# Kernel tuning notes

Hardware: AMD Instinct MI355X
Metric: run time of the kernel (lower is better)

Reference implementation:

```python
import jax, jax.numpy as jnp
import numpy as np

BETA = 0.9
THR = 1.0
NUM_STEPS = 10


@jax.custom_vjp
def spike(x):
    # Heaviside forward, fast-sigmoid surrogate backward (slope=25)
    return (x > 0).astype(x.dtype)

def _spike_fwd(x):
    return spike(x), x

def _spike_bwd(x, g):
    return (g / (25.0 * jnp.abs(x) + 1.0) ** 2,)

spike.defvjp(_spike_fwd, _spike_bwd)


def setup_inputs() -> dict:
    key = jax.random.key(0)
    ks = jax.random.split(key, 5)
    B = 65536
    x = jax.random.normal(ks[0], (B, 1, 16, 16), dtype=jnp.float32)
    conv_w = jax.random.normal(ks[1], (8, 1, 3, 3), dtype=jnp.float32) * 0.3
    conv_b = jax.random.normal(ks[2], (8,), dtype=jnp.float32) * 0.1
    fc_w = jax.random.normal(ks[3], (2, 2048), dtype=jnp.float32) * 0.05
    fc_b = jax.random.normal(ks[4], (2,), dtype=jnp.float32) * 0.1
    return {"x": x, "conv_w": conv_w, "conv_b": conv_b, "fc_w": fc_w, "fc_b": fc_b}


def reference(x, conv_w, conv_b, fc_w, fc_b):
    B = x.shape[0]
    # conv1(x) is loop-invariant (x is fed at every step) -> hoist
    cur1 = jax.lax.conv_general_dilated(
        x, conv_w, window_strides=(1, 1), padding="SAME",
        dimension_numbers=("NCHW", "OIHW", "NCHW"),
    ) + conv_b[None, :, None, None]  # [B, 8, 16, 16]

    def step(carry, _):
        mem1, mem2, acc = carry
        # snntorch Leaky: reset (detached) from previous mem, subtract mechanism
        reset1 = jax.lax.stop_gradient((mem1 > THR).astype(mem1.dtype))
        mem1 = BETA * mem1 + cur1 - reset1 * THR
        spk1 = spike(mem1 - THR)
        flat = spk1.reshape(B, -1)  # [B, 2048]
        cur2 = flat @ fc_w.T + fc_b  # [B, 2]
        reset2 = jax.lax.stop_gradient((mem2 > THR).astype(mem2.dtype))
        mem2 = BETA * mem2 + cur2 - reset2 * THR
        spk2 = spike(mem2 - THR)
        return (mem1, mem2, acc + spk2), None

    init = (
        jnp.zeros((B, 8, 16, 16), dtype=x.dtype),
        jnp.zeros((B, 2), dtype=x.dtype),
        jnp.zeros((B, 2), dtype=x.dtype),
    )
    (mem1, mem2, sum_out), _ = jax.lax.scan(step, init, None, length=NUM_STEPS)
    return sum_out
```

## Files before the change

### kernel.cpp

```cpp
#include <hip/hip_runtime.h>

#define NSTEP 10

__device__ __forceinline__ void load_row(const float* __restrict__ p, float* r) {
    const float4* q = reinterpret_cast<const float4*>(p);
    float4 a = q[0], b = q[1], c = q[2], d = q[3];
    r[0]=a.x;  r[1]=a.y;  r[2]=a.z;  r[3]=a.w;
    r[4]=b.x;  r[5]=b.y;  r[6]=b.z;  r[7]=b.w;
    r[8]=c.x;  r[9]=c.y;  r[10]=c.z; r[11]=c.w;
    r[12]=d.x; r[13]=d.y; r[14]=d.z; r[15]=d.w;
}

__global__ __launch_bounds__(256) void snn_fused_f64(
    const float* __restrict__ x,
    const float* __restrict__ conv_w,
    const float* __restrict__ conv_b,
    const float* __restrict__ fc_w,
    const float* __restrict__ fc_b,
    float* __restrict__ out,
    int B)
{
    __shared__ float2 fcw[2048];
    for (int j = threadIdx.x; j < 2048; j += 256)
        fcw[j] = make_float2(fc_w[j], fc_w[2048 + j]);
    __syncthreads();

    const int g  = blockIdx.x * 256 + threadIdx.x;
    const int b  = g >> 3;
    const int ch = g & 7;
    if (b >= B) return;

    double cw[9];
    #pragma unroll
    for (int k = 0; k < 9; ++k) cw[k] = (double)conv_w[ch * 9 + k];
    const double cb = (double)conv_b[ch];

    const float* xb = x + (size_t)b * 256;

    double sx[NSTEP], sy[NSTEP];
    #pragma unroll
    for (int t = 0; t < NSTEP; ++t) { sx[t] = 0.0; sy[t] = 0.0; }

    float r0[16], r1[16], r2[16];
    #pragma unroll
    for (int k = 0; k < 16; ++k) r0[k] = 0.f;
    load_row(xb, r1);
    load_row(xb + 16, r2);

    for (int y = 0; y < 16; ++y) {
        const int jbase = ch * 256 + y * 16;
        #pragma unroll
        for (int xx = 0; xx < 16; ++xx) {
            double c = cb;
            if (xx > 0) {
                c = fma(cw[0], (double)r0[xx - 1], c);
                c = fma(cw[3], (double)r1[xx - 1], c);
                c = fma(cw[6], (double)r2[xx - 1], c);
            }
            c = fma(cw[1], (double)r0[xx], c);
            c = fma(cw[4], (double)r1[xx], c);
            c = fma(cw[7], (double)r2[xx], c);
            if (xx < 15) {
                c = fma(cw[2], (double)r0[xx + 1], c);
                c = fma(cw[5], (double)r1[xx + 1], c);
                c = fma(cw[8], (double)r2[xx + 1], c);
            }
            const float2 w01 = fcw[jbase + xx];
            const double w0 = (double)w01.x;
            const double w1 = (double)w01.y;
            const double cm1 = c - 1.0;
            double mem = 0.0;
            bool spk = false;
            #pragma unroll
            for (int t = 0; t < NSTEP; ++t) {
                mem = fma(0.9, mem, spk ? cm1 : c);
                spk = mem > 1.0;
                sx[t] += spk ? w0 : 0.0;
                sy[t] += spk ? w1 : 0.0;
            }
        }
        #pragma unroll
        for (int k = 0; k < 16; ++k) { r0[k] = r1[k]; r1[k] = r2[k]; }
        if (y < 14) {
            load_row(xb + (y + 2) * 16, r2);
        } else {
            #pragma unroll
            for (int k = 0; k < 16; ++k) r2[k] = 0.f;
        }
    }

    #pragma unroll
    for (int t = 0; t < NSTEP; ++t) {
        sx[t] += __shfl_xor(sx[t], 1);
        sy[t] += __shfl_xor(sy[t], 1);
        sx[t] += __shfl_xor(sx[t], 2);
        sy[t] += __shfl_xor(sy[t], 2);
        sx[t] += __shfl_xor(sx[t], 4);
        sy[t] += __shfl_xor(sy[t], 4);
    }

    if (ch == 0) {
        const double fb0 = (double)fc_b[0];
        const double fb1 = (double)fc_b[1];
        double m0 = 0.0, m1 = 0.0, p0 = 0.0, p1 = 0.0;
        float a0 = 0.f, a1 = 0.f;
        #pragma unroll
        for (int t = 0; t < NSTEP; ++t) {
            m0 = fma(0.9, m0, (sx[t] + fb0) - p0);
            m1 = fma(0.9, m1, (sy[t] + fb1) - p1);
            p0 = (m0 > 1.0) ? 1.0 : 0.0;
            p1 = (m1 > 1.0) ? 1.0 : 0.0;
            a0 += (float)p0;
            a1 += (float)p1;
        }
        reinterpret_cast<float2*>(out)[b] = make_float2(a0, a1);
    }
}

extern "C" void kernel_launch(void* const* d_in, const int* in_sizes, int n_in,
                              void* d_out, int out_size, void* d_ws, size_t ws_size,
                              hipStream_t stream) {
    const float* x      = (const float*)d_in[0];
    const float* conv_w = (const float*)d_in[1];
    const float* conv_b = (const float*)d_in[2];
    const float* fc_w   = (const float*)d_in[3];
    const float* fc_b   = (const float*)d_in[4];
    float* out = (float*)d_out;

    const int B = in_sizes[0] / 256;
    const int threads = B * 8;
    const int blocks = (threads + 255) / 256;
    snn_fused_f64<<<blocks, 256, 0, stream>>>(x, conv_w, conv_b, fc_w, fc_b, out, B);
}
```

Measured before the change: 501.1 us.

## Run conv and membrane recurrence in fp32 with fp64 fallback near threshold

Moves the 3x3 conv and the 10-step membrane recurrence from fp64 to fp32, tracking a per-pixel error bound from the absolute-value sums. Pixels whose membrane comes within that bound of the threshold are flagged and recomputed in fp64 afterwards, and any differing spike bits are corrected in the fp64 accumulators. FC weights are pre-converted to double in padded shared memory so the per-step accumulation becomes a plain fma. This cuts fp64 ALU work but adds extra fp32 bound arithmetic, a rarely taken divergent fallback path, and higher register and shared-memory pressure.

```diff
diff --git a/kernel.cpp b/kernel.cpp
--- a/kernel.cpp
+++ b/kernel.cpp
@@ -1,6 +1,7 @@
 #include <hip/hip_runtime.h>
 
 #define NSTEP 10
+#define EPS32 5.9604645e-8f
 
 __device__ __forceinline__ void load_row(const float* __restrict__ p, float* r) {
     const float4* q = reinterpret_cast<const float4*>(p);
@@ -11,7 +12,7 @@
     r[12]=d.x; r[13]=d.y; r[14]=d.z; r[15]=d.w;
 }
 
-__global__ __launch_bounds__(256) void snn_fused_f64(
+__global__ __launch_bounds__(256) void snn_fused_fast(
     const float* __restrict__ x,
     const float* __restrict__ conv_w,
     const float* __restrict__ conv_b,
@@ -20,9 +21,11 @@
     float* __restrict__ out,
     int B)
 {
-    __shared__ float2 fcw[2048];
-    for (int j = threadIdx.x; j < 2048; j += 256)
-        fcw[j] = make_float2(fc_w[j], fc_w[2048 + j]);
+    __shared__ double2 fcwd[8 * 257];
+    for (int j = threadIdx.x; j < 2048; j += 256) {
+        const int c8 = j >> 8, idx = j & 255;
+        fcwd[c8 * 257 + idx] = make_double2((double)fc_w[j], (double)fc_w[2048 + j]);
+    }
     __syncthreads();
 
     const int g  = blockIdx.x * 256 + threadIdx.x;
@@ -30,12 +33,13 @@
     const int ch = g & 7;
     if (b >= B) return;
 
-    double cw[9];
-    #pragma unroll
-    for (int k = 0; k < 9; ++k) cw[k] = (double)conv_w[ch * 9 + k];
-    const double cb = (double)conv_b[ch];
+    float cw[9], aw[9];
+    #pragma unroll
+    for (int k = 0; k < 9; ++k) { cw[k] = conv_w[ch * 9 + k]; aw[k] = fabsf(cw[k]); }
+    const float cb = conv_b[ch];
 
     const float* xb = x + (size_t)b * 256;
+    const double2* fcw_ch = &fcwd[ch * 257];
 
     double sx[NSTEP], sy[NSTEP];
     #pragma unroll
@@ -48,37 +52,110 @@
     load_row(xb + 16, r2);
 
     for (int y = 0; y < 16; ++y) {
-        const int jbase = ch * 256 + y * 16;
+        unsigned rowflag = 0;
         #pragma unroll
         for (int xx = 0; xx < 16; ++xx) {
-            double c = cb;
+            float cf = cb;
+            float sa = fabsf(cb);
             if (xx > 0) {
-                c = fma(cw[0], (double)r0[xx - 1], c);
-                c = fma(cw[3], (double)r1[xx - 1], c);
-                c = fma(cw[6], (double)r2[xx - 1], c);
-            }
-            c = fma(cw[1], (double)r0[xx], c);
-            c = fma(cw[4], (double)r1[xx], c);
-            c = fma(cw[7], (double)r2[xx], c);
+                cf = fmaf(cw[0], r0[xx-1], cf); sa = fmaf(aw[0], fabsf(r0[xx-1]), sa);
+                cf = fmaf(cw[3], r1[xx-1], cf); sa = fmaf(aw[3], fabsf(r1[xx-1]), sa);
+                cf = fmaf(cw[6], r2[xx-1], cf); sa = fmaf(aw[6], fabsf(r2[xx-1]), sa);
+            }
+            cf = fmaf(cw[1], r0[xx], cf); sa = fmaf(aw[1], fabsf(r0[xx]), sa);
+            cf = fmaf(cw[4], r1[xx], cf); sa = fmaf(aw[4], fabsf(r1[xx]), sa);
+            cf = fmaf(cw[7], r2[xx], cf); sa = fmaf(aw[7], fabsf(r2[xx]), sa);
             if (xx < 15) {
-                c = fma(cw[2], (double)r0[xx + 1], c);
-                c = fma(cw[5], (double)r1[xx + 1], c);
-                c = fma(cw[8], (double)r2[xx + 1], c);
-            }
-            const float2 w01 = fcw[jbase + xx];
-            const double w0 = (double)w01.x;
-            const double w1 = (double)w01.y;
-            const double cm1 = c - 1.0;
-            double mem = 0.0;
+                cf = fmaf(cw[2], r0[xx+1], cf); sa = fmaf(aw[2], fabsf(r0[xx+1]), sa);
+                cf = fmaf(cw[5], r1[xx+1], cf); sa = fmaf(aw[5], fabsf(r1[xx+1]), sa);
+                cf = fmaf(cw[8], r2[xx+1], cf); sa = fmaf(aw[8], fabsf(r2[xx+1]), sa);
+            }
+            const double2 wd = fcw_ch[y * 16 + xx];
+            const float cm1f = cf - 1.0f;
+            const float Am    = fmaxf(fabsf(cf), fabsf(cm1f));
+            const float delta = fmaf(9.5367432e-6f, sa, fmaf(7.6293945e-6f, Am, 9.5367432e-7f));
+
+            float memf = 0.f, mn = 1e30f;
             bool spk = false;
             #pragma unroll
             for (int t = 0; t < NSTEP; ++t) {
-                mem = fma(0.9, mem, spk ? cm1 : c);
-                spk = mem > 1.0;
-                sx[t] += spk ? w0 : 0.0;
-                sy[t] += spk ? w1 : 0.0;
-            }
-        }
+                memf = fmaf(0.9f, memf, spk ? cm1f : cf);
+                const float sd = memf - 1.0f;
+                spk = sd > 0.0f;
+                mn = fminf(mn, fabsf(sd));
+                const double spkd = spk ? 1.0 : 0.0;
+                sx[t] = fma(spkd, wd.x, sx[t]);
+                sy[t] = fma(spkd, wd.y, sy[t]);
+            }
+            if (mn < delta) rowflag |= (1u << xx);
+        }
+
+        if (__builtin_expect(rowflag != 0, 0)) {
+            while (rowflag) {
+                const int xx = __builtin_ctz(rowflag);
+                rowflag &= rowflag - 1;
+                float v[3][3];
+                #pragma unroll
+                for (int ky = 0; ky < 3; ++ky) {
+                    const int ry = y + ky - 1;
+                    #pragma unroll
+                    for (int kx = 0; kx < 3; ++kx) {
+                        const int rx = xx + kx - 1;
+                        v[ky][kx] = (ry >= 0 && ry < 16 && rx >= 0 && rx < 16)
+                                        ? xb[ry * 16 + rx] : 0.f;
+                    }
+                }
+                float cf = cb;
+                cf = fmaf(cw[0], v[0][0], cf); cf = fmaf(cw[3], v[1][0], cf); cf = fmaf(cw[6], v[2][0], cf);
+                cf = fmaf(cw[1], v[0][1], cf); cf = fmaf(cw[4], v[1][1], cf); cf = fmaf(cw[7], v[2][1], cf);
+                cf = fmaf(cw[2], v[0][2], cf); cf = fmaf(cw[5], v[1][2], cf); cf = fmaf(cw[8], v[2][2], cf);
+                const float cm1f = cf - 1.0f;
+                unsigned b32 = 0;
+                {
+                    float memf = 0.f; bool spk = false;
+                    #pragma unroll
+                    for (int t = 0; t < NSTEP; ++t) {
+                        memf = fmaf(0.9f, memf, spk ? cm1f : cf);
+                        spk = (memf - 1.0f) > 0.0f;
+                        b32 |= (unsigned)spk << t;
+                    }
+                }
+                double c64 = (double)cb;
+                c64 = fma((double)cw[0], (double)v[0][0], c64);
+                c64 = fma((double)cw[3], (double)v[1][0], c64);
+                c64 = fma((double)cw[6], (double)v[2][0], c64);
+                c64 = fma((double)cw[1], (double)v[0][1], c64);
+                c64 = fma((double)cw[4], (double)v[1][1], c64);
+                c64 = fma((double)cw[7], (double)v[2][1], c64);
+                c64 = fma((double)cw[2], (double)v[0][2], c64);
+                c64 = fma((double)cw[5], (double)v[1][2], c64);
+                c64 = fma((double)cw[8], (double)v[2][2], c64);
+                const double cm164 = c64 - 1.0;
+                unsigned b64m = 0;
+                {
+                    double mem = 0.0; bool sk = false;
+                    #pragma unroll
+                    for (int t = 0; t < NSTEP; ++t) {
+                        mem = fma(0.9, mem, sk ? cm164 : c64);
+                        sk = mem > 1.0;
+                        b64m |= (unsigned)sk << t;
+                    }
+                }
+                if (b64m != b32) {
+                    const double2 wd = fcw_ch[y * 16 + xx];
+                    #pragma unroll
+                    for (int t = 0; t < NSTEP; ++t) {
+                        const int d = (int)((b64m >> t) & 1u) - (int)((b32 >> t) & 1u);
+                        if (d != 0) {
+                            const double dd = (double)d;
+                            sx[t] = fma(dd, wd.x, sx[t]);
+                            sy[t] = fma(dd, wd.y, sy[t]);
+                        }
+                    }
+                }
+            }
+        }
+
         #pragma unroll
         for (int k = 0; k < 16; ++k) { r0[k] = r1[k]; r1[k] = r2[k]; }
         if (y < 14) {
@@ -130,5 +207,5 @@
     const int B = in_sizes[0] / 256;
     const int threads = B * 8;
     const int blocks = (threads + 255) / 256;
-    snn_fused_f64<<<blocks, 256, 0, stream>>>(x, conv_w, conv_b, fc_w, fc_b, out, B);
+    snn_fused_fast<<<blocks, 256, 0, stream>>>(x, conv_w, conv_b, fc_w, fc_b, out, B);
 }
```

Result: slower. 576.0 us (+14.9%).
